# Kernel tuning notes

Hardware: AMD Instinct MI355X
Metric: run time of the kernel (lower is better)

Reference implementation:

```python
import jax, jax.numpy as jnp
import numpy as np

TOP_K = 2  # init arg top_k
EPS = 1e-9


def setup_inputs() -> dict:
    key = jax.random.key(0)
    ks = jax.random.split(key, 5)
    B, L, D, E, H, G = 2, 2048, 2048, 8, 2048, 256
    s = lambda k, sh, fan: jax.random.normal(k, sh, jnp.float32) / np.sqrt(fan)
    return {
        "x": jax.random.normal(ks[0], (B, L, D), jnp.float32),
        "wg1": s(ks[1], (D, G), D),
        "wg2": s(ks[2], (G, E), G),
        "w1": s(ks[3], (E, D, H), D),
        "w2": s(ks[4], (E, H, D), H),
    }


def reference(x, wg1, wg2, w1, w2):
    B, L, D = x.shape
    xf = x.reshape(-1, D)                                  # [T, D]
    T = xf.shape[0]

    # --- top-k gating (mlp gate) ---
    logits = jax.nn.gelu(xf @ wg1) @ wg2                   # [T, E]
    probs = jax.nn.softmax(logits, axis=-1)                # [T, E]
    top_vals, top_idx = jax.lax.top_k(probs, TOP_K)        # [T, k]
    # dense gate matrix: gate weight where expert selected, else 0
    gates = jnp.zeros_like(probs).at[jnp.arange(T)[:, None], top_idx].set(top_vals)  # [T, E]

    # --- grouped expert FFN (dense-equivalent of gather/grouped-GEMM/scatter) ---
    h = jax.nn.gelu(jnp.einsum('td,edh->teh', xf, w1))     # [T, E, H]
    gh = h * gates[:, :, None]                             # fold gates in (linear in h)
    y = jnp.einsum('teh,ehd->td', gh, w2).reshape(B, L, D)

    # --- mutual-information aux loss: -H(E) + H(E|X) ---
    p_mean = probs.mean(axis=0)                            # [E]
    loss = jnp.sum(p_mean * jnp.log(p_mean + EPS)) \
         - jnp.mean(jnp.sum(probs * jnp.log(probs + EPS), axis=-1))
    return y, loss
```

## Files before the change

### kernel.cpp

```cpp
#include <hip/hip_runtime.h>

#define T_TOK 4096
#define NROWS_MAX 10240
#define MAX_TILES 72

typedef float  fv4  __attribute__((ext_vector_type(4)));
typedef __bf16 bv4  __attribute__((ext_vector_type(4)));
typedef __bf16 bv8  __attribute__((ext_vector_type(8)));

#define CTRL_OFF     0
#define ROWTOK_OFF   4096
#define ROWGATE_OFF  45056
#define TOPIDX_OFF   86016
#define TOPVAL_OFF   118784
#define G_OFF        151552
#define XB_OFF       4345856
#define W1T_OFF      21123072
#define W2T_OFF      88231936
#define HBUF_OFF     155340800

struct Ctrl {
    int   counts[8];
    float psum[8];
    float entsum;
    int   ntiles;
    int   off[8];
    int   tile_e[MAX_TILES];
    int   tile_r0[MAX_TILES];
};

__device__ __forceinline__ float gelu_f(float x) {
    float x3 = x * x * x;
    return 0.5f * x * (1.0f + tanhf(0.7978845608028654f * (x + 0.044715f * x3)));
}

__device__ __forceinline__ void g2l16(const void* gptr, void* lptr) {
    __builtin_amdgcn_global_load_lds(
        (const __attribute__((address_space(1))) void*)gptr,
        (__attribute__((address_space(3))) void*)lptr, 16, 0, 0);
}

__global__ __launch_bounds__(256) void transpose_cvt(
    const float* __restrict__ w1, const float* __restrict__ w2,
    __bf16* __restrict__ w1t, __bf16* __restrict__ w2t)
{
    int b    = blockIdx.x;
    int mat  = b >> 10;
    int tile = b & 1023;
    int trow = tile >> 5, tcol = tile & 31;
    const float* src = (mat < 8) ? (w1 + (size_t)mat * 4194304)
                                 : (w2 + (size_t)(mat - 8) * 4194304);
    __bf16* dst = (mat < 8) ? (w1t + (size_t)mat * 4194304)
                            : (w2t + (size_t)(mat - 8) * 4194304);
    __shared__ float tileS[64][65];
    int tid = threadIdx.x;
    int c = tid & 63, r4 = tid >> 6;
#pragma unroll
    for (int u = 0; u < 16; u++) {
        int rr = u * 4 + r4;
        tileS[rr][c] = src[(size_t)(trow * 64 + rr) * 2048 + tcol * 64 + c];
    }
    __syncthreads();
    int c2 = (tid & 31) * 2, r8 = tid >> 5;
#pragma unroll
    for (int u = 0; u < 8; u++) {
        int rr = u * 8 + r8;
        __bf16 v0 = (__bf16)tileS[c2][rr];
        __bf16 v1 = (__bf16)tileS[c2 + 1][rr];
        size_t o = (size_t)(tcol * 64 + rr) * 2048 + trow * 64 + c2;
        dst[o]     = v0;
        dst[o + 1] = v1;
    }
}

__global__ __launch_bounds__(256) void cvt_x_kernel(const float* __restrict__ x,
                                                    __bf16* __restrict__ xb)
{
    size_t idx = ((size_t)blockIdx.x * 256 + threadIdx.x) * 4;
    fv4 v = *(const fv4*)(x + idx);
    bv4 o;
#pragma unroll
    for (int u = 0; u < 4; u++) o[u] = (__bf16)v[u];
    *(bv4*)(xb + idx) = o;
}

__global__ __launch_bounds__(256) void gating_gemm(const float* __restrict__ x,
                                                   const float* __restrict__ wg1,
                                                   float* __restrict__ g)
{
    __shared__ float As[16][68];
    __shared__ float Bs[16][68];
    int tid = threadIdx.x;
    int tx = tid & 15, ty = tid >> 4;
    int mb = blockIdx.x, nb = blockIdx.y;
    float acc[4][4];
#pragma unroll
    for (int u = 0; u < 4; u++)
#pragma unroll
        for (int v = 0; v < 4; v++) acc[u][v] = 0.f;

    int r  = tid >> 2, kq = tid & 3;
    int kb = tid >> 4, n4 = (tid & 15) * 4;
    const float* gx = x + (size_t)(mb * 64 + r) * 2048 + kq * 4;
    const float* gw = wg1 + nb * 64 + n4;

    for (int k0 = 0; k0 < 2048; k0 += 16) {
        fv4 av = *(const fv4*)(gx + k0);
        fv4 bv = *(const fv4*)(gw + (size_t)(k0 + kb) * 256);
        __syncthreads();
#pragma unroll
        for (int u = 0; u < 4; u++) As[kq * 4 + u][r] = av[u];
        *(fv4*)&Bs[kb][n4] = bv;
        __syncthreads();
#pragma unroll
        for (int k = 0; k < 16; k++) {
            fv4 a = *(const fv4*)&As[k][ty * 4];
            fv4 b = *(const fv4*)&Bs[k][tx * 4];
#pragma unroll
            for (int u = 0; u < 4; u++)
#pragma unroll
                for (int v = 0; v < 4; v++) acc[u][v] += a[u] * b[v];
        }
    }
#pragma unroll
    for (int u = 0; u < 4; u++) {
        int row = mb * 64 + ty * 4 + u;
#pragma unroll
        for (int v = 0; v < 4; v++)
            g[(size_t)row * 256 + nb * 64 + tx * 4 + v] = gelu_f(acc[u][v]);
    }
}

__global__ __launch_bounds__(256) void gate_kernel(
    const float* __restrict__ g, const float* __restrict__ wg2,
    Ctrl* __restrict__ ctrl, int* __restrict__ topidx, float* __restrict__ topval)
{
    __shared__ float wg2s[256 * 9];
    __shared__ float psum_s[8];
    __shared__ float ent_s;
    __shared__ int   cnt_s[8];
    int tid = threadIdx.x;
    for (int i = tid; i < 2048; i += 256) {
        int k = i >> 3, e = i & 7;
        wg2s[k * 9 + e] = wg2[i];
    }
    if (tid < 8) { psum_s[tid] = 0.f; cnt_s[tid] = 0; }
    if (tid == 8) ent_s = 0.f;
    __syncthreads();

    int lane = tid & 63, wv = tid >> 6;
    int t = blockIdx.x * 4 + wv;
    fv4 g4 = *(const fv4*)&g[(size_t)t * 256 + lane * 4];
    float part[8];
#pragma unroll
    for (int e = 0; e < 8; e++) part[e] = 0.f;
#pragma unroll
    for (int u = 0; u < 4; u++) {
        int k = lane * 4 + u;
        float gv = g4[u];
#pragma unroll
        for (int e = 0; e < 8; e++) part[e] += gv * wg2s[k * 9 + e];
    }
#pragma unroll
    for (int e = 0; e < 8; e++)
        for (int off = 32; off; off >>= 1) part[e] += __shfl_xor(part[e], off);

    if (lane == 0) {
        float mx = part[0];
#pragma unroll
        for (int e = 1; e < 8; e++) mx = fmaxf(mx, part[e]);
        float p[8], Z = 0.f;
#pragma unroll
        for (int e = 0; e < 8; e++) { p[e] = expf(part[e] - mx); Z += p[e]; }
        float rz = 1.f / Z;
#pragma unroll
        for (int e = 0; e < 8; e++) p[e] *= rz;
        int i0 = 0;
#pragma unroll
        for (int e = 1; e < 8; e++) if (part[e] > part[i0]) i0 = e;
        int i1 = (i0 == 0) ? 1 : 0;
#pragma unroll
        for (int e = 0; e < 8; e++)
            if (e != i0 && part[e] > part[i1]) i1 = e;
        topidx[2 * t]     = i0;
        topidx[2 * t + 1] = i1;
        topval[2 * t]     = p[i0];
        topval[2 * t + 1] = p[i1];
        float ent = 0.f;
#pragma unroll
        for (int e = 0; e < 8; e++) ent += p[e] * logf(p[e] + 1e-9f);
#pragma unroll
        for (int e = 0; e < 8; e++) atomicAdd(&psum_s[e], p[e]);
        atomicAdd(&ent_s, ent);
        atomicAdd(&cnt_s[i0], 1);
        atomicAdd(&cnt_s[i1], 1);
    }
    __syncthreads();
    if (tid < 8)                    atomicAdd(&ctrl->psum[tid], psum_s[tid]);
    else if (tid == 8)              atomicAdd(&ctrl->entsum, ent_s);
    else if (tid >= 16 && tid < 24) atomicAdd(&ctrl->counts[tid - 16], cnt_s[tid - 16]);
}

__global__ __launch_bounds__(256) void route_kernel(
    Ctrl* __restrict__ ctrl, const int* __restrict__ topidx,
    const float* __restrict__ topval, int* __restrict__ rowtok,
    float* __restrict__ rowgate)
{
    __shared__ int cur[8];
    __shared__ int offs_s[8];
    int tid = threadIdx.x;
    if (tid == 0) {
        int off = 0, nt = 0;
        for (int e = 0; e < 8; e++) {
            offs_s[e]    = off;
            ctrl->off[e] = off;
            int c = ctrl->counts[e];
            for (int m = 0; m < c; m += 128) {
                ctrl->tile_e[nt]  = e;
                ctrl->tile_r0[nt] = off + m;
                nt++;
            }
            off += ((c + 127) >> 7) << 7;
        }
        ctrl->ntiles = nt;
    }
    if (tid < 8) cur[tid] = 0;
    __syncthreads();
    for (int t = tid; t < T_TOK; t += 256) {
#pragma unroll
        for (int k = 0; k < 2; k++) {
            int e = topidx[2 * t + k];
            int p = atomicAdd(&cur[e], 1);
            int row = offs_s[e] + p;
            rowtok[row]  = t;
            rowgate[row] = topval[2 * t + k];
        }
    }
}

#define NBLK 1152

template <bool IS_FFN1>
__global__ __launch_bounds__(256, 4) void gemm_grouped(
    const __bf16* __restrict__ A,
    const __bf16* __restrict__ Bt,
    const Ctrl* __restrict__ ctrl,
    const int* __restrict__ rowtok,
    const float* __restrict__ rowgate,
    __bf16* __restrict__ hbuf,
    float* __restrict__ y)
{
    __shared__ __bf16 As[128 * 32];
    __shared__ __bf16 Bs[128 * 32];

    const int tid  = threadIdx.x;
    const int lane = tid & 63, w = tid >> 6;
    const int wm = w >> 1, wn = w & 1;
    const int l15 = lane & 15;
    const int kswz8 = (((lane >> 4) ^ ((lane >> 1) & 3)) << 3);
    const int stb = w * 512;
    const int srow = tid >> 2;
    const int sk8  = (((tid & 3) ^ ((tid >> 3) & 3)) << 3);

    int ntiles = ctrl->ntiles;
    int nitems = ntiles << 4;
    int item = (blockIdx.x & 7) * (NBLK / 8) + (blockIdx.x >> 3);
    if (item >= nitems) return;

    int tl = item >> 4, nb = item & 15;
    int e  = ctrl->tile_e[tl];
    int r0 = ctrl->tile_r0[tl];

    int rA0, rA1;
    if constexpr (IS_FFN1) {
        rA0 = rowtok[r0 + srow];
        rA1 = rowtok[r0 + 64 + srow];
    } else {
        rA0 = r0 + srow;
        rA1 = rA0 + 64;
    }
    const __bf16* pa0 = A + (size_t)rA0 * 2048 + sk8;
    const __bf16* pa1 = A + (size_t)rA1 * 2048 + sk8;
    const __bf16* pb0 = Bt + ((size_t)e * 2048 + nb * 128 + srow) * 2048 + sk8;
    const __bf16* pb1 = pb0 + (size_t)64 * 2048;

    fv4 acc[4][4];
#pragma unroll
    for (int i = 0; i < 4; i++)
#pragma unroll
        for (int j = 0; j < 4; j++) acc[i][j] = (fv4)0.0f;

    for (int k = 0; k < 2048; k += 32) {
        __syncthreads();
        g2l16(pa0 + k, As + stb);
        g2l16(pa1 + k, As + 2048 + stb);
        g2l16(pb0 + k, Bs + stb);
        g2l16(pb1 + k, Bs + 2048 + stb);
        __syncthreads();

        bv8 aF[4], bF[4];
#pragma unroll
        for (int i = 0; i < 4; i++)
            aF[i] = *(const bv8*)&As[(wm * 64 + i * 16 + l15) * 32 + kswz8];
#pragma unroll
        for (int j = 0; j < 4; j++)
            bF[j] = *(const bv8*)&Bs[(wn * 64 + j * 16 + l15) * 32 + kswz8];
#pragma unroll
        for (int i = 0; i < 4; i++)
#pragma unroll
            for (int j = 0; j < 4; j++)
                acc[i][j] = __builtin_amdgcn_mfma_f32_16x16x32_bf16(
                    aF[i], bF[j], acc[i][j], 0, 0, 0);
    }

    int colb = nb * 128 + wn * 64 + l15;
    int rb   = r0 + wm * 64 + (lane >> 4) * 4;
#pragma unroll
    for (int i = 0; i < 4; i++) {
#pragma unroll
        for (int rr = 0; rr < 4; rr++) {
            int rg = rb + i * 16 + rr;
            if constexpr (IS_FFN1) {
                float gate = rowgate[rg];
                size_t ho = (size_t)rg * 2048;
#pragma unroll
                for (int j = 0; j < 4; j++)
                    hbuf[ho + colb + j * 16] = (__bf16)(gelu_f(acc[i][j][rr]) * gate);
            } else {
                size_t yo = (size_t)rowtok[rg] * 2048;
#pragma unroll
                for (int j = 0; j < 4; j++)
                    atomicAdd(&y[yo + colb + j * 16], acc[i][j][rr]);
            }
        }
    }
}

__global__ __launch_bounds__(64) void loss_kernel(const Ctrl* __restrict__ ctrl,
                                                  float* __restrict__ out)
{
    if (threadIdx.x == 0) {
        float a = 0.f;
#pragma unroll
        for (int e = 0; e < 8; e++) {
            float pm = ctrl->psum[e] * (1.0f / 4096.0f);
            a += pm * logf(pm + 1e-9f);
        }
        out[0] = a - ctrl->entsum * (1.0f / 4096.0f);
    }
}

extern "C" void kernel_launch(void* const* d_in, const int* in_sizes, int n_in,
                              void* d_out, int out_size, void* d_ws, size_t ws_size,
                              hipStream_t stream)
{
    const float* x   = (const float*)d_in[0];
    const float* wg1 = (const float*)d_in[1];
    const float* wg2 = (const float*)d_in[2];
    const float* w1  = (const float*)d_in[3];
    const float* w2  = (const float*)d_in[4];
    float* out = (float*)d_out;

    char* ws = (char*)d_ws;
    Ctrl*   ctrl    = (Ctrl*)(ws + CTRL_OFF);
    int*    rowtok  = (int*)(ws + ROWTOK_OFF);
    float*  rowgate = (float*)(ws + ROWGATE_OFF);
    int*    topidx  = (int*)(ws + TOPIDX_OFF);
    float*  topval  = (float*)(ws + TOPVAL_OFF);
    float*  g       = (float*)(ws + G_OFF);
    __bf16* xb      = (__bf16*)(ws + XB_OFF);
    __bf16* w1t     = (__bf16*)(ws + W1T_OFF);
    __bf16* w2t     = (__bf16*)(ws + W2T_OFF);
    __bf16* hbuf    = (__bf16*)(ws + HBUF_OFF);

    hipMemsetAsync(ws + CTRL_OFF, 0, 4096, stream);
    hipMemsetAsync(ws + ROWTOK_OFF, 0, 81920, stream);
    hipMemsetAsync(d_out, 0, (size_t)out_size * sizeof(float), stream);

    transpose_cvt<<<16384, 256, 0, stream>>>(w1, w2, w1t, w2t);
    cvt_x_kernel<<<8192, 256, 0, stream>>>(x, xb);
    gating_gemm<<<dim3(64, 4), 256, 0, stream>>>(x, wg1, g);
    gate_kernel<<<1024, 256, 0, stream>>>(g, wg2, ctrl, topidx, topval);
    route_kernel<<<1, 256, 0, stream>>>(ctrl, topidx, topval, rowtok, rowgate);
    gemm_grouped<true><<<NBLK, 256, 0, stream>>>(xb, w1t, ctrl, rowtok, rowgate, hbuf, nullptr);
    gemm_grouped<false><<<NBLK, 256, 0, stream>>>(hbuf, w2t, ctrl, rowtok, rowgate, nullptr, out);
    loss_kernel<<<1, 64, 0, stream>>>(ctrl, out + 8388608);
}
```

Baseline: 815.0 us.

## Split-K gating GEMM, vectorize transpose stores, deepen grouped GEMM K tile

Three independent changes. The gating GEMM now uses 128-row tiles and splits K into four chunks, with atomicAdd accumulation into a zeroed buffer and GELU moved into gate_kernel. This raises the block count from 256 to 512 and fills more CUs. The transpose kernel writes 4 bf16 values per store instead of scalar pairs. The grouped expert GEMM stages a K=64 slice per iteration with a wider XOR swizzle, halving the barrier count per tile at the cost of doubling LDS use, which may reduce occupancy.

```diff
diff --git a/kernel.cpp b/kernel.cpp
--- a/kernel.cpp
+++ b/kernel.cpp
@@ -61,15 +61,16 @@
         tileS[rr][c] = src[(size_t)(trow * 64 + rr) * 2048 + tcol * 64 + c];
     }
     __syncthreads();
-    int c2 = (tid & 31) * 2, r8 = tid >> 5;
-#pragma unroll
-    for (int u = 0; u < 8; u++) {
-        int rr = u * 8 + r8;
-        __bf16 v0 = (__bf16)tileS[c2][rr];
-        __bf16 v1 = (__bf16)tileS[c2 + 1][rr];
-        size_t o = (size_t)(tcol * 64 + rr) * 2048 + trow * 64 + c2;
-        dst[o]     = v0;
-        dst[o + 1] = v1;
+    int c4 = (tid & 15) * 4, r16 = tid >> 4;
+#pragma unroll
+    for (int u = 0; u < 4; u++) {
+        int rr = u * 16 + r16;
+        bv4 o;
+        o[0] = (__bf16)tileS[c4][rr];
+        o[1] = (__bf16)tileS[c4 + 1][rr];
+        o[2] = (__bf16)tileS[c4 + 2][rr];
+        o[3] = (__bf16)tileS[c4 + 3][rr];
+        *(bv4*)&dst[(size_t)(tcol * 64 + rr) * 2048 + trow * 64 + c4] = o;
     }
 }
 
@@ -88,46 +89,59 @@
                                                    const float* __restrict__ wg1,
                                                    float* __restrict__ g)
 {
-    __shared__ float As[16][68];
+    __shared__ float As[16][132];
     __shared__ float Bs[16][68];
     int tid = threadIdx.x;
+    int bid = blockIdx.x;
+    int mb = bid & 31;
+    int nb = (bid >> 5) & 3;
+    int ks = bid >> 7;
     int tx = tid & 15, ty = tid >> 4;
-    int mb = blockIdx.x, nb = blockIdx.y;
-    float acc[4][4];
-#pragma unroll
-    for (int u = 0; u < 4; u++)
+    float acc[8][4];
+#pragma unroll
+    for (int u = 0; u < 8; u++)
 #pragma unroll
         for (int v = 0; v < 4; v++) acc[u][v] = 0.f;
 
-    int r  = tid >> 2, kq = tid & 3;
+    int r  = tid >> 1, kq = (tid & 1) * 8;
     int kb = tid >> 4, n4 = (tid & 15) * 4;
-    const float* gx = x + (size_t)(mb * 64 + r) * 2048 + kq * 4;
-    const float* gw = wg1 + nb * 64 + n4;
-
-    for (int k0 = 0; k0 < 2048; k0 += 16) {
-        fv4 av = *(const fv4*)(gx + k0);
-        fv4 bv = *(const fv4*)(gw + (size_t)(k0 + kb) * 256);
+    const float* gx = x + (size_t)(mb * 128 + r) * 2048 + ks * 512 + kq;
+    const float* gw = wg1 + (size_t)(ks * 512 + kb) * 256 + nb * 64 + n4;
+
+    for (int k0 = 0; k0 < 512; k0 += 16) {
+        fv4 a0 = *(const fv4*)(gx + k0);
+        fv4 a1 = *(const fv4*)(gx + k0 + 4);
+        fv4 bv = *(const fv4*)(gw + (size_t)k0 * 256);
         __syncthreads();
 #pragma unroll
-        for (int u = 0; u < 4; u++) As[kq * 4 + u][r] = av[u];
+        for (int u = 0; u < 4; u++) {
+            As[kq + u][r]     = a0[u];
+            As[kq + 4 + u][r] = a1[u];
+        }
         *(fv4*)&Bs[kb][n4] = bv;
         __syncthreads();
 #pragma unroll
         for (int k = 0; k < 16; k++) {
-            fv4 a = *(const fv4*)&As[k][ty * 4];
-            fv4 b = *(const fv4*)&Bs[k][tx * 4];
+            fv4 b  = *(const fv4*)&Bs[k][tx * 4];
+            fv4 a0v = *(const fv4*)&As[k][ty * 8];
+            fv4 a1v = *(const fv4*)&As[k][ty * 8 + 4];
 #pragma unroll
             for (int u = 0; u < 4; u++)
 #pragma unroll
-                for (int v = 0; v < 4; v++) acc[u][v] += a[u] * b[v];
-        }
-    }
-#pragma unroll
-    for (int u = 0; u < 4; u++) {
-        int row = mb * 64 + ty * 4 + u;
+                for (int v = 0; v < 4; v++) {
+                    acc[u][v]     += a0v[u] * b[v];
+                    acc[u + 4][v] += a1v[u] * b[v];
+                }
+        }
+    }
+#pragma unroll
+    for (int u = 0; u < 8; u++) {
+        int row = mb * 128 + ty * 8 + ((u < 4) ? u : (u - 4) + 4);
 #pragma unroll
         for (int v = 0; v < 4; v++)
-            g[(size_t)row * 256 + nb * 64 + tx * 4 + v] = gelu_f(acc[u][v]);
+            atomicAdd(&g[(size_t)(mb * 128 + ty * 8 + u) * 256 + nb * 64 + tx * 4 + v],
+                      acc[u][v]);
+        (void)row;
     }
 }
 
@@ -157,7 +171,7 @@
 #pragma unroll
     for (int u = 0; u < 4; u++) {
         int k = lane * 4 + u;
-        float gv = g4[u];
+        float gv = gelu_f(g4[u]);
 #pragma unroll
         for (int e = 0; e < 8; e++) part[e] += gv * wg2s[k * 9 + e];
     }
@@ -250,17 +264,18 @@
     __bf16* __restrict__ hbuf,
     float* __restrict__ y)
 {
-    __shared__ __bf16 As[128 * 32];
-    __shared__ __bf16 Bs[128 * 32];
+    __shared__ __bf16 As[128 * 64];
+    __shared__ __bf16 Bs[128 * 64];
 
     const int tid  = threadIdx.x;
     const int lane = tid & 63, w = tid >> 6;
     const int wm = w >> 1, wn = w & 1;
     const int l15 = lane & 15;
-    const int kswz8 = (((lane >> 4) ^ ((lane >> 1) & 3)) << 3);
     const int stb = w * 512;
-    const int srow = tid >> 2;
-    const int sk8  = (((tid & 3) ^ ((tid >> 3) & 3)) << 3);
+    const int srow = tid >> 3;
+    const int sk8  = (((tid & 7) ^ ((tid >> 3) & 7)) << 3);
+    const int kc0  = (((lane >> 4)) ^ (l15 & 7)) << 3;
+    const int kc1  = (((lane >> 4) | 4) ^ (l15 & 7)) << 3;
 
     int ntiles = ctrl->ntiles;
     int nitems = ntiles << 4;
@@ -271,18 +286,26 @@
     int e  = ctrl->tile_e[tl];
     int r0 = ctrl->tile_r0[tl];
 
-    int rA0, rA1;
+    int rA0, rA1, rA2, rA3;
     if constexpr (IS_FFN1) {
         rA0 = rowtok[r0 + srow];
-        rA1 = rowtok[r0 + 64 + srow];
+        rA1 = rowtok[r0 + 32 + srow];
+        rA2 = rowtok[r0 + 64 + srow];
+        rA3 = rowtok[r0 + 96 + srow];
     } else {
         rA0 = r0 + srow;
-        rA1 = rA0 + 64;
+        rA1 = rA0 + 32;
+        rA2 = rA0 + 64;
+        rA3 = rA0 + 96;
     }
     const __bf16* pa0 = A + (size_t)rA0 * 2048 + sk8;
     const __bf16* pa1 = A + (size_t)rA1 * 2048 + sk8;
+    const __bf16* pa2 = A + (size_t)rA2 * 2048 + sk8;
+    const __bf16* pa3 = A + (size_t)rA3 * 2048 + sk8;
     const __bf16* pb0 = Bt + ((size_t)e * 2048 + nb * 128 + srow) * 2048 + sk8;
-    const __bf16* pb1 = pb0 + (size_t)64 * 2048;
+    const __bf16* pb1 = pb0 + (size_t)32 * 2048;
+    const __bf16* pb2 = pb0 + (size_t)64 * 2048;
+    const __bf16* pb3 = pb0 + (size_t)96 * 2048;
 
     fv4 acc[4][4];
 #pragma unroll
@@ -290,27 +313,35 @@
 #pragma unroll
         for (int j = 0; j < 4; j++) acc[i][j] = (fv4)0.0f;
 
-    for (int k = 0; k < 2048; k += 32) {
+    for (int k = 0; k < 2048; k += 64) {
         __syncthreads();
         g2l16(pa0 + k, As + stb);
         g2l16(pa1 + k, As + 2048 + stb);
+        g2l16(pa2 + k, As + 4096 + stb);
+        g2l16(pa3 + k, As + 6144 + stb);
         g2l16(pb0 + k, Bs + stb);
         g2l16(pb1 + k, Bs + 2048 + stb);
+        g2l16(pb2 + k, Bs + 4096 + stb);
+        g2l16(pb3 + k, Bs + 6144 + stb);
         __syncthreads();
 
-        bv8 aF[4], bF[4];
-#pragma unroll
-        for (int i = 0; i < 4; i++)
-            aF[i] = *(const bv8*)&As[(wm * 64 + i * 16 + l15) * 32 + kswz8];
-#pragma unroll
-        for (int j = 0; j < 4; j++)
-            bF[j] = *(const bv8*)&Bs[(wn * 64 + j * 16 + l15) * 32 + kswz8];
-#pragma unroll
-        for (int i = 0; i < 4; i++)
+#pragma unroll
+        for (int ks = 0; ks < 2; ks++) {
+            const int kc = ks ? kc1 : kc0;
+            bv8 aF[4], bF[4];
+#pragma unroll
+            for (int i = 0; i < 4; i++)
+                aF[i] = *(const bv8*)&As[(wm * 64 + i * 16 + l15) * 64 + kc];
 #pragma unroll
             for (int j = 0; j < 4; j++)
-                acc[i][j] = __builtin_amdgcn_mfma_f32_16x16x32_bf16(
-                    aF[i], bF[j], acc[i][j], 0, 0, 0);
+                bF[j] = *(const bv8*)&Bs[(wn * 64 + j * 16 + l15) * 64 + kc];
+#pragma unroll
+            for (int i = 0; i < 4; i++)
+#pragma unroll
+                for (int j = 0; j < 4; j++)
+                    acc[i][j] = __builtin_amdgcn_mfma_f32_16x16x32_bf16(
+                        aF[i], bF[j], acc[i][j], 0, 0, 0);
+        }
     }
 
     int colb = nb * 128 + wn * 64 + l15;
@@ -375,11 +406,12 @@
 
     hipMemsetAsync(ws + CTRL_OFF, 0, 4096, stream);
     hipMemsetAsync(ws + ROWTOK_OFF, 0, 81920, stream);
+    hipMemsetAsync(ws + G_OFF, 0, 4194304, stream);
     hipMemsetAsync(d_out, 0, (size_t)out_size * sizeof(float), stream);
 
     transpose_cvt<<<16384, 256, 0, stream>>>(w1, w2, w1t, w2t);
     cvt_x_kernel<<<8192, 256, 0, stream>>>(x, xb);
-    gating_gemm<<<dim3(64, 4), 256, 0, stream>>>(x, wg1, g);
+    gating_gemm<<<512, 256, 0, stream>>>(x, wg1, g);
     gate_kernel<<<1024, 256, 0, stream>>>(g, wg2, ctrl, topidx, topval);
     route_kernel<<<1, 256, 0, stream>>>(ctrl, topidx, topval, rowtok, rowgate);
     gemm_grouped<true><<<NBLK, 256, 0, stream>>>(xb, w1t, ctrl, rowtok, rowgate, hbuf, nullptr);
```

Measured after the change: 839.0 us. 1.03x slower.
